# Kernel tuning notes

Measured on AMD Instinct MI355X. Metric: run time of the kernel, lower is better.

Reference implementation:

```python
import jax, jax.numpy as jnp
import numpy as np

IN, U = 256, 512
UNFOLDS = 6

def setup_inputs() -> dict:
    key = jax.random.key(0)
    ks = jax.random.split(key, 16)
    B = 512
    inputs = jax.random.normal(ks[0], (B, IN), dtype=jnp.float32)
    state = jax.random.normal(ks[1], (B, U), dtype=jnp.float32)
    # parameters, initialized like the torch module
    sensory_mu = jax.random.uniform(ks[2], (IN, U), minval=0.3, maxval=0.8)
    sensory_sigma = jax.random.uniform(ks[3], (IN, U), minval=3.0, maxval=8.0)
    sensory_W = jax.random.uniform(ks[4], (IN, U), minval=0.01, maxval=1.0)
    sensory_erev = (2.0 * jax.random.randint(ks[5], (IN, U), 0, 2).astype(jnp.float32) - 1.0)
    mu = jax.random.uniform(ks[6], (U, U), minval=0.3, maxval=0.8)
    sigma = jax.random.uniform(ks[7], (U, U), minval=3.0, maxval=8.0)
    W = jax.random.uniform(ks[8], (U, U), minval=0.01, maxval=1.0)
    erev = (2.0 * jax.random.randint(ks[9], (U, U), 0, 2).astype(jnp.float32) - 1.0)
    vleak = jax.random.uniform(ks[10], (U,), minval=-0.2, maxval=0.2)
    gleak = jnp.ones((U,), dtype=jnp.float32)   # gleak_init_min == max == 1.0
    cm_t = jnp.full((U,), 0.5, dtype=jnp.float32)  # cm_init_min == max == 0.5
    input_w = jnp.ones((IN,), dtype=jnp.float32)
    input_b = jnp.zeros((IN,), dtype=jnp.float32)
    return dict(inputs=inputs, state=state, input_w=input_w, input_b=input_b,
                sensory_mu=sensory_mu, sensory_sigma=sensory_sigma,
                sensory_W=sensory_W, sensory_erev=sensory_erev,
                mu=mu, sigma=sigma, W=W, erev=erev,
                vleak=vleak, gleak=gleak, cm_t=cm_t)

def _syn_sigmoid(v, mu, sigma):
    # v: [B, N] -> [B, N, 1]; mu, sigma: [N, M]; result [B, N, M]
    return jax.nn.sigmoid(sigma * (v[..., None] - mu))

def reference(inputs, state, input_w, input_b, sensory_mu, sensory_sigma,
              sensory_W, sensory_erev, mu, sigma, W, erev, vleak, gleak, cm_t):
    # Affine input mapping
    x = inputs * input_w + input_b                       # [B, IN]
    # sensory synapses (computed once)
    sens_act = sensory_W * _syn_sigmoid(x, sensory_mu, sensory_sigma)  # [B, IN, U]
    w_num_s = jnp.sum(sens_act * sensory_erev, axis=1)   # [B, U]
    w_den_s = jnp.sum(sens_act, axis=1)                  # [B, U]
    # semi-implicit ODE unfold (6 fixed steps)
    v_pre = state
    for _ in range(UNFOLDS):
        w_act = W * _syn_sigmoid(v_pre, mu, sigma)       # [B, U, U]
        w_num = jnp.sum(w_act * erev, axis=1) + w_num_s  # [B, U]
        w_den = jnp.sum(w_act, axis=1) + w_den_s         # [B, U]
        numerator = cm_t * v_pre + gleak * vleak + w_num
        denominator = cm_t + gleak + w_den
        v_pre = numerator / denominator
    return v_pre  # module returns (next_state, next_state); both identical
```

## Files before the change

kernel.cpp:

```cpp
#include <hip/hip_runtime.h>

#define IN_DIM 256
#define U_DIM  512
#define L2E    1.44269504088896340736f

__global__ void k_fuse(const float* __restrict__ mu, const float* __restrict__ sigma,
                       const float* __restrict__ W, const float* __restrict__ erev,
                       float2* __restrict__ sm2, float* __restrict__ wep, int n) {
    int i = blockIdx.x * blockDim.x + threadIdx.x;
    if (i < n) {
        float s = sigma[i] * L2E;
        sm2[i] = make_float2(s, mu[i] * s);
        wep[i] = W[i] * erev[i];
    }
}

__global__ __launch_bounds__(512, 4) void k_sensory(
    const float* __restrict__ inputs, const float* __restrict__ input_w,
    const float* __restrict__ input_b,
    const float* __restrict__ smu, const float* __restrict__ ssig,
    const float* __restrict__ sW, const float* __restrict__ serev,
    float* __restrict__ wnum_s, float* __restrict__ wden_s) {
    __shared__ __align__(16) float xs[8 * IN_DIM];
    __shared__ float red[8 * 8 * 64 * 2];
    const int tid = threadIdx.x;
    const int b0 = blockIdx.x * 8;
    const int u0 = blockIdx.y * 64;

    #pragma unroll
    for (int k = 0; k < 4; ++k) {
        int idx = tid + k * 512;
        int r = idx >> 8, i = idx & 255;
        xs[idx] = fmaf(inputs[(b0 + r) * IN_DIM + i], input_w[i], input_b[i]);
    }
    __syncthreads();

    const int ul = tid & 63;
    const int strip = tid >> 6;
    const int u = u0 + ul;
    float nacc[8], dacc[8];
    #pragma unroll
    for (int r = 0; r < 8; ++r) { nacc[r] = 0.f; dacc[r] = 0.f; }

    const int i0 = strip * 32;
    for (int ic = 0; ic < 32; ic += 4) {
        const int i = i0 + ic;
        float sgl[4], msl[4], w_[4], wer[4];
        #pragma unroll
        for (int j = 0; j < 4; ++j) {
            const int pi = (i + j) * U_DIM + u;
            float m = smu[pi];
            float sg = ssig[pi] * L2E;
            float w = sW[pi];
            sgl[j] = sg; msl[j] = m * sg; w_[j] = w; wer[j] = w * serev[pi];
        }
        #pragma unroll
        for (int r = 0; r < 8; ++r) {
            const float4 x4 = *reinterpret_cast<const float4*>(&xs[r * IN_DIM + i]);
            const float xv[4] = { x4.x, x4.y, x4.z, x4.w };
            #pragma unroll
            for (int j = 0; j < 4; ++j) {
                float e = __builtin_amdgcn_exp2f(fmaf(-sgl[j], xv[j], msl[j]));
                float p = __builtin_amdgcn_rcpf(1.f + e);
                nacc[r] = fmaf(wer[j], p, nacc[r]);
                dacc[r] = fmaf(w_[j], p, dacc[r]);
            }
        }
    }
    #pragma unroll
    for (int r = 0; r < 8; ++r) {
        red[(((strip * 8 + r) * 64) + ul) * 2 + 0] = nacc[r];
        red[(((strip * 8 + r) * 64) + ul) * 2 + 1] = dacc[r];
    }
    __syncthreads();
    {
        const int r = tid >> 6, uu = tid & 63;
        float n = 0.f, d = 0.f;
        #pragma unroll
        for (int s = 0; s < 8; ++s) {
            n += red[(((s * 8 + r) * 64) + uu) * 2 + 0];
            d += red[(((s * 8 + r) * 64) + uu) * 2 + 1];
        }
        wnum_s[(b0 + r) * U_DIM + (u0 + uu)] = n;
        wden_s[(b0 + r) * U_DIM + (u0 + uu)] = d;
    }
}

__global__ __launch_bounds__(512, 4) void k_unfold(
    const float* __restrict__ vin,
    const float2* __restrict__ sm2, const float* __restrict__ wep,
    const float* __restrict__ wnum_s, const float* __restrict__ wden_s,
    const float* __restrict__ vleak, const float* __restrict__ gleak,
    const float* __restrict__ cm,
    float* __restrict__ vout) {
    __shared__ __align__(16) float vs[8 * U_DIM];
    __shared__ float red[8 * 8 * 64 * 2];
    const int tid = threadIdx.x;
    const int b0 = blockIdx.x * 8;
    const int u0 = blockIdx.y * 64;

    #pragma unroll
    for (int k = 0; k < 8; ++k) {
        int idx = tid + k * 512;
        vs[idx] = vin[b0 * U_DIM + idx];
    }
    __syncthreads();

    const int ul = tid & 63;
    const int strip = tid >> 6;
    const int u = u0 + ul;
    float nacc[8], dacc[8];
    #pragma unroll
    for (int r = 0; r < 8; ++r) { nacc[r] = 0.f; dacc[r] = 0.f; }

    const int i0 = strip * 64;
    for (int ic = 0; ic < 64; ic += 4) {
        const int i = i0 + ic;
        float2 p0 = sm2[(i + 0) * U_DIM + u];
        float2 p1 = sm2[(i + 1) * U_DIM + u];
        float2 p2 = sm2[(i + 2) * U_DIM + u];
        float2 p3 = sm2[(i + 3) * U_DIM + u];
        float we0 = wep[(i + 0) * U_DIM + u];
        float we1 = wep[(i + 1) * U_DIM + u];
        float we2 = wep[(i + 2) * U_DIM + u];
        float we3 = wep[(i + 3) * U_DIM + u];
        float w0 = fabsf(we0), w1 = fabsf(we1), w2 = fabsf(we2), w3 = fabsf(we3);
        #pragma unroll
        for (int r = 0; r < 8; ++r) {
            const float4 v4 = *reinterpret_cast<const float4*>(&vs[r * U_DIM + i]);
            {
                float e = __builtin_amdgcn_exp2f(fmaf(-p0.x, v4.x, p0.y));
                float p = __builtin_amdgcn_rcpf(1.f + e);
                nacc[r] = fmaf(we0, p, nacc[r]); dacc[r] = fmaf(w0, p, dacc[r]);
            }
            {
                float e = __builtin_amdgcn_exp2f(fmaf(-p1.x, v4.y, p1.y));
                float p = __builtin_amdgcn_rcpf(1.f + e);
                nacc[r] = fmaf(we1, p, nacc[r]); dacc[r] = fmaf(w1, p, dacc[r]);
            }
            {
                float e = __builtin_amdgcn_exp2f(fmaf(-p2.x, v4.z, p2.y));
                float p = __builtin_amdgcn_rcpf(1.f + e);
                nacc[r] = fmaf(we2, p, nacc[r]); dacc[r] = fmaf(w2, p, dacc[r]);
            }
            {
                float e = __builtin_amdgcn_exp2f(fmaf(-p3.x, v4.w, p3.y));
                float p = __builtin_amdgcn_rcpf(1.f + e);
                nacc[r] = fmaf(we3, p, nacc[r]); dacc[r] = fmaf(w3, p, dacc[r]);
            }
        }
    }
    #pragma unroll
    for (int r = 0; r < 8; ++r) {
        red[(((strip * 8 + r) * 64) + ul) * 2 + 0] = nacc[r];
        red[(((strip * 8 + r) * 64) + ul) * 2 + 1] = dacc[r];
    }
    __syncthreads();
    {
        const int r = tid >> 6, uu = tid & 63;
        float n = 0.f, d = 0.f;
        #pragma unroll
        for (int s = 0; s < 8; ++s) {
            n += red[(((s * 8 + r) * 64) + uu) * 2 + 0];
            d += red[(((s * 8 + r) * 64) + uu) * 2 + 1];
        }
        const int gu = u0 + uu, gb = b0 + r;
        float vold = vs[r * U_DIM + gu];
        float gl = gleak[gu], c = cm[gu];
        float num = fmaf(c, vold, fmaf(gl, vleak[gu], n + wnum_s[gb * U_DIM + gu]));
        float den = c + gl + d + wden_s[gb * U_DIM + gu];
        vout[gb * U_DIM + gu] = num / den;
    }
}

__global__ __launch_bounds__(512) void k_mono(
    const float* __restrict__ inputs, const float* __restrict__ state,
    const float* __restrict__ input_w, const float* __restrict__ input_b,
    const float* __restrict__ smu, const float* __restrict__ ssig,
    const float* __restrict__ sW, const float* __restrict__ serev,
    const float* __restrict__ mu, const float* __restrict__ sigma,
    const float* __restrict__ W, const float* __restrict__ erev,
    const float* __restrict__ vleak, const float* __restrict__ gleak,
    const float* __restrict__ cm, float* __restrict__ out) {
    __shared__ float xs[IN_DIM];
    __shared__ float vsh[U_DIM];
    const int b = blockIdx.x, u = threadIdx.x;
    if (u < IN_DIM) xs[u] = fmaf(inputs[b * IN_DIM + u], input_w[u], input_b[u]);
    vsh[u] = state[b * U_DIM + u];
    __syncthreads();
    float ns = 0.f, ds = 0.f;
    for (int i = 0; i < IN_DIM; ++i) {
        int pi = i * U_DIM + u;
        float e = __builtin_amdgcn_exp2f((smu[pi] - xs[i]) * (ssig[pi] * L2E));
        float p = __builtin_amdgcn_rcpf(1.f + e);
        float a = sW[pi] * p;
        ns = fmaf(a, serev[pi], ns);
        ds += a;
    }
    const float c = cm[u], gl = gleak[u], glvl = gl * vleak[u];
    for (int t = 0; t < 6; ++t) {
        float n = ns, d = ds;
        for (int i = 0; i < U_DIM; ++i) {
            int pi = i * U_DIM + u;
            float e = __builtin_amdgcn_exp2f((mu[pi] - vsh[i]) * (sigma[pi] * L2E));
            float p = __builtin_amdgcn_rcpf(1.f + e);
            float a = W[pi] * p;
            n = fmaf(a, erev[pi], n);
            d += a;
        }
        float vn = (fmaf(c, vsh[u], glvl) + n) / (c + gl + d);
        __syncthreads();
        vsh[u] = vn;
        __syncthreads();
    }
    out[b * U_DIM + u] = vsh[u];
}

extern "C" void kernel_launch(void* const* d_in, const int* in_sizes, int n_in,
                              void* d_out, int out_size, void* d_ws, size_t ws_size,
                              hipStream_t stream) {
    const float* inputs  = (const float*)d_in[0];
    const float* state   = (const float*)d_in[1];
    const float* input_w = (const float*)d_in[2];
    const float* input_b = (const float*)d_in[3];
    const float* smu     = (const float*)d_in[4];
    const float* ssig    = (const float*)d_in[5];
    const float* sW      = (const float*)d_in[6];
    const float* serev   = (const float*)d_in[7];
    const float* mu      = (const float*)d_in[8];
    const float* sigma   = (const float*)d_in[9];
    const float* W       = (const float*)d_in[10];
    const float* erev    = (const float*)d_in[11];
    const float* vleak   = (const float*)d_in[12];
    const float* gleak   = (const float*)d_in[13];
    const float* cm      = (const float*)d_in[14];
    float* out = (float*)d_out;

    const int B = in_sizes[1] / U_DIM;
    const size_t BU = (size_t)B * U_DIM;
    const size_t UU = (size_t)U_DIM * U_DIM;
    const size_t need = (3 * BU + 3 * UU) * sizeof(float);

    if (ws_size >= need) {
        float* f      = (float*)d_ws;
        float* wnum_s = f;
        float* wden_s = f + BU;
        float* vbuf   = f + 2 * BU;
        float2* sm2   = (float2*)(f + 3 * BU);
        float* wep    = f + 3 * BU + 2 * UU;

        k_fuse<<<(int)((UU + 255) / 256), 256, 0, stream>>>(mu, sigma, W, erev, sm2, wep, (int)UU);
        dim3 grid(B / 8, U_DIM / 64);
        k_sensory<<<grid, 512, 0, stream>>>(inputs, input_w, input_b,
                                            smu, ssig, sW, serev, wnum_s, wden_s);
        const float* vin = state;
        float* pong[2] = { vbuf, out };
        for (int t = 0; t < 6; ++t) {
            float* vo = pong[t & 1];
            k_unfold<<<grid, 512, 0, stream>>>(vin, sm2, wep,
                                               wnum_s, wden_s, vleak, gleak, cm, vo);
            vin = vo;
        }
    } else {
        k_mono<<<B, U_DIM, 0, stream>>>(inputs, state, input_w, input_b,
                                        smu, ssig, sW, serev, mu, sigma, W, erev,
                                        vleak, gleak, cm, out);
    }
}
```

Before: 220.2 us.

## Pack synapse params into float4, shrink batch tile to 4, raise occupancy

Precomputes both the recurrent and the sensory synapse parameters into interleaved float4 records (scaled sigma, mu*sigma, W*erev, W), so each inner step issues one 16-byte load. The sensory kernel now reads these records instead of recomputing them from four arrays. Both compute kernels drop their batch tile from 8 to 4 rows and raise the launch bounds to 8 blocks per SM, for more blocks and occupancy. The cost is parameter reuse across rows halving, so twice as many parameter loads per unit of work, plus a larger workspace and a bigger preprocessing kernel.

```diff
diff --git a/kernel.cpp b/kernel.cpp
--- a/kernel.cpp
+++ b/kernel.cpp
@@ -6,29 +6,36 @@
 
 __global__ void k_fuse(const float* __restrict__ mu, const float* __restrict__ sigma,
                        const float* __restrict__ W, const float* __restrict__ erev,
-                       float2* __restrict__ sm2, float* __restrict__ wep, int n) {
+                       const float* __restrict__ smu, const float* __restrict__ ssig,
+                       const float* __restrict__ sW, const float* __restrict__ serev,
+                       float4* __restrict__ pf4, float4* __restrict__ sf4) {
     int i = blockIdx.x * blockDim.x + threadIdx.x;
-    if (i < n) {
+    const int UU = U_DIM * U_DIM;
+    const int SU = IN_DIM * U_DIM;
+    if (i < UU) {
         float s = sigma[i] * L2E;
-        sm2[i] = make_float2(s, mu[i] * s);
-        wep[i] = W[i] * erev[i];
-    }
-}
-
-__global__ __launch_bounds__(512, 4) void k_sensory(
+        float w = W[i];
+        pf4[i] = make_float4(s, mu[i] * s, w * erev[i], w);
+    } else if (i < UU + SU) {
+        int j = i - UU;
+        float s = ssig[j] * L2E;
+        float w = sW[j];
+        sf4[j] = make_float4(s, smu[j] * s, w * serev[j], w);
+    }
+}
+
+__global__ __launch_bounds__(512, 8) void k_sensory(
     const float* __restrict__ inputs, const float* __restrict__ input_w,
-    const float* __restrict__ input_b,
-    const float* __restrict__ smu, const float* __restrict__ ssig,
-    const float* __restrict__ sW, const float* __restrict__ serev,
+    const float* __restrict__ input_b, const float4* __restrict__ sf4,
     float* __restrict__ wnum_s, float* __restrict__ wden_s) {
-    __shared__ __align__(16) float xs[8 * IN_DIM];
-    __shared__ float red[8 * 8 * 64 * 2];
+    __shared__ __align__(16) float xs[4 * IN_DIM];
+    __shared__ float red[8 * 4 * 64 * 2];
     const int tid = threadIdx.x;
-    const int b0 = blockIdx.x * 8;
+    const int b0 = blockIdx.x * 4;
     const int u0 = blockIdx.y * 64;
 
     #pragma unroll
-    for (int k = 0; k < 4; ++k) {
+    for (int k = 0; k < 2; ++k) {
         int idx = tid + k * 512;
         int r = idx >> 8, i = idx & 255;
         xs[idx] = fmaf(inputs[(b0 + r) * IN_DIM + i], input_w[i], input_b[i]);
@@ -38,131 +45,128 @@
     const int ul = tid & 63;
     const int strip = tid >> 6;
     const int u = u0 + ul;
-    float nacc[8], dacc[8];
-    #pragma unroll
-    for (int r = 0; r < 8; ++r) { nacc[r] = 0.f; dacc[r] = 0.f; }
+    float nacc[4], dacc[4];
+    #pragma unroll
+    for (int r = 0; r < 4; ++r) { nacc[r] = 0.f; dacc[r] = 0.f; }
 
     const int i0 = strip * 32;
     for (int ic = 0; ic < 32; ic += 4) {
         const int i = i0 + ic;
-        float sgl[4], msl[4], w_[4], wer[4];
-        #pragma unroll
-        for (int j = 0; j < 4; ++j) {
-            const int pi = (i + j) * U_DIM + u;
-            float m = smu[pi];
-            float sg = ssig[pi] * L2E;
-            float w = sW[pi];
-            sgl[j] = sg; msl[j] = m * sg; w_[j] = w; wer[j] = w * serev[pi];
-        }
-        #pragma unroll
-        for (int r = 0; r < 8; ++r) {
+        float4 q0 = sf4[(i + 0) * U_DIM + u];
+        float4 q1 = sf4[(i + 1) * U_DIM + u];
+        float4 q2 = sf4[(i + 2) * U_DIM + u];
+        float4 q3 = sf4[(i + 3) * U_DIM + u];
+        #pragma unroll
+        for (int r = 0; r < 4; ++r) {
             const float4 x4 = *reinterpret_cast<const float4*>(&xs[r * IN_DIM + i]);
-            const float xv[4] = { x4.x, x4.y, x4.z, x4.w };
-            #pragma unroll
-            for (int j = 0; j < 4; ++j) {
-                float e = __builtin_amdgcn_exp2f(fmaf(-sgl[j], xv[j], msl[j]));
-                float p = __builtin_amdgcn_rcpf(1.f + e);
-                nacc[r] = fmaf(wer[j], p, nacc[r]);
-                dacc[r] = fmaf(w_[j], p, dacc[r]);
-            }
-        }
-    }
-    #pragma unroll
-    for (int r = 0; r < 8; ++r) {
-        red[(((strip * 8 + r) * 64) + ul) * 2 + 0] = nacc[r];
-        red[(((strip * 8 + r) * 64) + ul) * 2 + 1] = dacc[r];
-    }
-    __syncthreads();
-    {
+            {
+                float e = __builtin_amdgcn_exp2f(fmaf(-q0.x, x4.x, q0.y));
+                float p = __builtin_amdgcn_rcpf(1.f + e);
+                nacc[r] = fmaf(q0.z, p, nacc[r]); dacc[r] = fmaf(q0.w, p, dacc[r]);
+            }
+            {
+                float e = __builtin_amdgcn_exp2f(fmaf(-q1.x, x4.y, q1.y));
+                float p = __builtin_amdgcn_rcpf(1.f + e);
+                nacc[r] = fmaf(q1.z, p, nacc[r]); dacc[r] = fmaf(q1.w, p, dacc[r]);
+            }
+            {
+                float e = __builtin_amdgcn_exp2f(fmaf(-q2.x, x4.z, q2.y));
+                float p = __builtin_amdgcn_rcpf(1.f + e);
+                nacc[r] = fmaf(q2.z, p, nacc[r]); dacc[r] = fmaf(q2.w, p, dacc[r]);
+            }
+            {
+                float e = __builtin_amdgcn_exp2f(fmaf(-q3.x, x4.w, q3.y));
+                float p = __builtin_amdgcn_rcpf(1.f + e);
+                nacc[r] = fmaf(q3.z, p, nacc[r]); dacc[r] = fmaf(q3.w, p, dacc[r]);
+            }
+        }
+    }
+    #pragma unroll
+    for (int r = 0; r < 4; ++r) {
+        red[(((strip * 4 + r) * 64) + ul) * 2 + 0] = nacc[r];
+        red[(((strip * 4 + r) * 64) + ul) * 2 + 1] = dacc[r];
+    }
+    __syncthreads();
+    if (tid < 4 * 64) {
         const int r = tid >> 6, uu = tid & 63;
         float n = 0.f, d = 0.f;
         #pragma unroll
         for (int s = 0; s < 8; ++s) {
-            n += red[(((s * 8 + r) * 64) + uu) * 2 + 0];
-            d += red[(((s * 8 + r) * 64) + uu) * 2 + 1];
+            n += red[(((s * 4 + r) * 64) + uu) * 2 + 0];
+            d += red[(((s * 4 + r) * 64) + uu) * 2 + 1];
         }
         wnum_s[(b0 + r) * U_DIM + (u0 + uu)] = n;
         wden_s[(b0 + r) * U_DIM + (u0 + uu)] = d;
     }
 }
 
-__global__ __launch_bounds__(512, 4) void k_unfold(
-    const float* __restrict__ vin,
-    const float2* __restrict__ sm2, const float* __restrict__ wep,
+__global__ __launch_bounds__(512, 8) void k_unfold(
+    const float* __restrict__ vin, const float4* __restrict__ pf4,
     const float* __restrict__ wnum_s, const float* __restrict__ wden_s,
     const float* __restrict__ vleak, const float* __restrict__ gleak,
-    const float* __restrict__ cm,
-    float* __restrict__ vout) {
-    __shared__ __align__(16) float vs[8 * U_DIM];
-    __shared__ float red[8 * 8 * 64 * 2];
+    const float* __restrict__ cm, float* __restrict__ vout) {
+    __shared__ __align__(16) float vs[4 * U_DIM];
+    __shared__ float red[8 * 4 * 64 * 2];
     const int tid = threadIdx.x;
-    const int b0 = blockIdx.x * 8;
+    const int b0 = blockIdx.x * 4;
     const int u0 = blockIdx.y * 64;
 
-    #pragma unroll
-    for (int k = 0; k < 8; ++k) {
-        int idx = tid + k * 512;
-        vs[idx] = vin[b0 * U_DIM + idx];
-    }
+    reinterpret_cast<float4*>(vs)[tid] =
+        reinterpret_cast<const float4*>(vin + (size_t)b0 * U_DIM)[tid];
     __syncthreads();
 
     const int ul = tid & 63;
     const int strip = tid >> 6;
     const int u = u0 + ul;
-    float nacc[8], dacc[8];
-    #pragma unroll
-    for (int r = 0; r < 8; ++r) { nacc[r] = 0.f; dacc[r] = 0.f; }
+    float nacc[4], dacc[4];
+    #pragma unroll
+    for (int r = 0; r < 4; ++r) { nacc[r] = 0.f; dacc[r] = 0.f; }
 
     const int i0 = strip * 64;
     for (int ic = 0; ic < 64; ic += 4) {
         const int i = i0 + ic;
-        float2 p0 = sm2[(i + 0) * U_DIM + u];
-        float2 p1 = sm2[(i + 1) * U_DIM + u];
-        float2 p2 = sm2[(i + 2) * U_DIM + u];
-        float2 p3 = sm2[(i + 3) * U_DIM + u];
-        float we0 = wep[(i + 0) * U_DIM + u];
-        float we1 = wep[(i + 1) * U_DIM + u];
-        float we2 = wep[(i + 2) * U_DIM + u];
-        float we3 = wep[(i + 3) * U_DIM + u];
-        float w0 = fabsf(we0), w1 = fabsf(we1), w2 = fabsf(we2), w3 = fabsf(we3);
-        #pragma unroll
-        for (int r = 0; r < 8; ++r) {
+        float4 q0 = pf4[(i + 0) * U_DIM + u];
+        float4 q1 = pf4[(i + 1) * U_DIM + u];
+        float4 q2 = pf4[(i + 2) * U_DIM + u];
+        float4 q3 = pf4[(i + 3) * U_DIM + u];
+        #pragma unroll
+        for (int r = 0; r < 4; ++r) {
             const float4 v4 = *reinterpret_cast<const float4*>(&vs[r * U_DIM + i]);
             {
-                float e = __builtin_amdgcn_exp2f(fmaf(-p0.x, v4.x, p0.y));
-                float p = __builtin_amdgcn_rcpf(1.f + e);
-                nacc[r] = fmaf(we0, p, nacc[r]); dacc[r] = fmaf(w0, p, dacc[r]);
-            }
-            {
-                float e = __builtin_amdgcn_exp2f(fmaf(-p1.x, v4.y, p1.y));
-                float p = __builtin_amdgcn_rcpf(1.f + e);
-                nacc[r] = fmaf(we1, p, nacc[r]); dacc[r] = fmaf(w1, p, dacc[r]);
-            }
-            {
-                float e = __builtin_amdgcn_exp2f(fmaf(-p2.x, v4.z, p2.y));
-                float p = __builtin_amdgcn_rcpf(1.f + e);
-                nacc[r] = fmaf(we2, p, nacc[r]); dacc[r] = fmaf(w2, p, dacc[r]);
-            }
-            {
-                float e = __builtin_amdgcn_exp2f(fmaf(-p3.x, v4.w, p3.y));
-                float p = __builtin_amdgcn_rcpf(1.f + e);
-                nacc[r] = fmaf(we3, p, nacc[r]); dacc[r] = fmaf(w3, p, dacc[r]);
-            }
-        }
-    }
-    #pragma unroll
-    for (int r = 0; r < 8; ++r) {
-        red[(((strip * 8 + r) * 64) + ul) * 2 + 0] = nacc[r];
-        red[(((strip * 8 + r) * 64) + ul) * 2 + 1] = dacc[r];
-    }
-    __syncthreads();
-    {
+                float e = __builtin_amdgcn_exp2f(fmaf(-q0.x, v4.x, q0.y));
+                float p = __builtin_amdgcn_rcpf(1.f + e);
+                nacc[r] = fmaf(q0.z, p, nacc[r]); dacc[r] = fmaf(q0.w, p, dacc[r]);
+            }
+            {
+                float e = __builtin_amdgcn_exp2f(fmaf(-q1.x, v4.y, q1.y));
+                float p = __builtin_amdgcn_rcpf(1.f + e);
+                nacc[r] = fmaf(q1.z, p, nacc[r]); dacc[r] = fmaf(q1.w, p, dacc[r]);
+            }
+            {
+                float e = __builtin_amdgcn_exp2f(fmaf(-q2.x, v4.z, q2.y));
+                float p = __builtin_amdgcn_rcpf(1.f + e);
+                nacc[r] = fmaf(q2.z, p, nacc[r]); dacc[r] = fmaf(q2.w, p, dacc[r]);
+            }
+            {
+                float e = __builtin_amdgcn_exp2f(fmaf(-q3.x, v4.w, q3.y));
+                float p = __builtin_amdgcn_rcpf(1.f + e);
+                nacc[r] = fmaf(q3.z, p, nacc[r]); dacc[r] = fmaf(q3.w, p, dacc[r]);
+            }
+        }
+    }
+    #pragma unroll
+    for (int r = 0; r < 4; ++r) {
+        red[(((strip * 4 + r) * 64) + ul) * 2 + 0] = nacc[r];
+        red[(((strip * 4 + r) * 64) + ul) * 2 + 1] = dacc[r];
+    }
+    __syncthreads();
+    if (tid < 4 * 64) {
         const int r = tid >> 6, uu = tid & 63;
         float n = 0.f, d = 0.f;
         #pragma unroll
         for (int s = 0; s < 8; ++s) {
-            n += red[(((s * 8 + r) * 64) + uu) * 2 + 0];
-            d += red[(((s * 8 + r) * 64) + uu) * 2 + 1];
+            n += red[(((s * 4 + r) * 64) + uu) * 2 + 0];
+            d += red[(((s * 4 + r) * 64) + uu) * 2 + 1];
         }
         const int gu = u0 + uu, gb = b0 + r;
         float vold = vs[r * U_DIM + gu];
@@ -239,26 +243,28 @@
     const int B = in_sizes[1] / U_DIM;
     const size_t BU = (size_t)B * U_DIM;
     const size_t UU = (size_t)U_DIM * U_DIM;
-    const size_t need = (3 * BU + 3 * UU) * sizeof(float);
+    const size_t SU = (size_t)IN_DIM * U_DIM;
+    const size_t need = (3 * BU + 4 * UU + 4 * SU) * sizeof(float);
 
     if (ws_size >= need) {
         float* f      = (float*)d_ws;
         float* wnum_s = f;
         float* wden_s = f + BU;
         float* vbuf   = f + 2 * BU;
-        float2* sm2   = (float2*)(f + 3 * BU);
-        float* wep    = f + 3 * BU + 2 * UU;
-
-        k_fuse<<<(int)((UU + 255) / 256), 256, 0, stream>>>(mu, sigma, W, erev, sm2, wep, (int)UU);
-        dim3 grid(B / 8, U_DIM / 64);
-        k_sensory<<<grid, 512, 0, stream>>>(inputs, input_w, input_b,
-                                            smu, ssig, sW, serev, wnum_s, wden_s);
+        float4* pf4   = (float4*)(f + 3 * BU);
+        float4* sf4   = (float4*)(f + 3 * BU + 4 * UU);
+
+        const int nfuse = (int)(UU + SU);
+        k_fuse<<<(nfuse + 255) / 256, 256, 0, stream>>>(mu, sigma, W, erev,
+                                                        smu, ssig, sW, serev, pf4, sf4);
+        dim3 grid(B / 4, U_DIM / 64);
+        k_sensory<<<grid, 512, 0, stream>>>(inputs, input_w, input_b, sf4, wnum_s, wden_s);
         const float* vin = state;
         float* pong[2] = { vbuf, out };
         for (int t = 0; t < 6; ++t) {
             float* vo = pong[t & 1];
-            k_unfold<<<grid, 512, 0, stream>>>(vin, sm2, wep,
-                                               wnum_s, wden_s, vleak, gleak, cm, vo);
+            k_unfold<<<grid, 512, 0, stream>>>(vin, pf4, wnum_s, wden_s,
+                                               vleak, gleak, cm, vo);
             vin = vo;
         }
     } else {
```

After: 223.1 us. About the same (+1.3%).

## Pack synapse parameters in pairs for packed-FP32 math and halve unit tile

Applied to the files above, without the earlier changes.

Preprocessing now interleaves parameters for two adjacent presynaptic rows into float4 records (negated scaled sigma, scaled mu, W*erev, W). This lets the inner loops issue one 16-byte load and use two-wide FMAs that can map to packed FP32 instructions. The sensory stage gets the same preprocessing, replacing its per-element parameter loads. Each block now covers 32 units with two strips per wave, combined by a cross-half shuffle before the shared reduction, which doubles the grid. The final division becomes an approximate reciprocal multiply, and the preprocessing pass writes more workspace.

```diff
diff --git a/kernel.cpp b/kernel.cpp
--- a/kernel.cpp
+++ b/kernel.cpp
@@ -4,28 +4,67 @@
 #define U_DIM  512
 #define L2E    1.44269504088896340736f
 
+typedef float f32x2 __attribute__((ext_vector_type(2)));
+typedef float f32x4 __attribute__((ext_vector_type(4)));
+
+__device__ __forceinline__ f32x2 vfma2(f32x2 a, f32x2 b, f32x2 c) {
+    return __builtin_elementwise_fma(a, b, c);
+}
+
 __global__ void k_fuse(const float* __restrict__ mu, const float* __restrict__ sigma,
                        const float* __restrict__ W, const float* __restrict__ erev,
-                       float2* __restrict__ sm2, float* __restrict__ wep, int n) {
-    int i = blockIdx.x * blockDim.x + threadIdx.x;
-    if (i < n) {
-        float s = sigma[i] * L2E;
-        sm2[i] = make_float2(s, mu[i] * s);
-        wep[i] = W[i] * erev[i];
-    }
-}
+                       const float* __restrict__ smu, const float* __restrict__ ssig,
+                       const float* __restrict__ sW, const float* __restrict__ serev,
+                       f32x4* __restrict__ rp4, f32x4* __restrict__ wp4,
+                       f32x4* __restrict__ sp4, f32x4* __restrict__ swp4) {
+    const int NR = (U_DIM / 2) * U_DIM;
+    const int NS = (IN_DIM / 2) * U_DIM;
+    int t = blockIdx.x * blockDim.x + threadIdx.x;
+    if (t < NR) {
+        const int u = t & (U_DIM - 1);
+        const int pr = t >> 9;
+        const int a = (2 * pr) * U_DIM + u, b = (2 * pr + 1) * U_DIM + u;
+        float s0 = sigma[a] * L2E, s1 = sigma[b] * L2E;
+        float w0 = W[a], w1 = W[b];
+        rp4[t] = (f32x4){ -s0, -s1, mu[a] * s0, mu[b] * s1 };
+        wp4[t] = (f32x4){ w0 * erev[a], w1 * erev[b], w0, w1 };
+    } else if (t < NR + NS) {
+        const int j = t - NR;
+        const int u = j & (U_DIM - 1);
+        const int pr = j >> 9;
+        const int a = (2 * pr) * U_DIM + u, b = (2 * pr + 1) * U_DIM + u;
+        float s0 = ssig[a] * L2E, s1 = ssig[b] * L2E;
+        float w0 = sW[a], w1 = sW[b];
+        sp4[j] = (f32x4){ -s0, -s1, smu[a] * s0, smu[b] * s1 };
+        swp4[j] = (f32x4){ w0 * serev[a], w1 * serev[b], w0, w1 };
+    }
+}
+
+#define PAIR_STEP(Q, WD, VP, NA, DA)                                               \
+    {                                                                              \
+        f32x2 t_ = vfma2((Q).xy, (VP), (Q).zw);                                    \
+        f32x2 e_;                                                                  \
+        e_.x = __builtin_amdgcn_exp2f(t_.x);                                       \
+        e_.y = __builtin_amdgcn_exp2f(t_.y);                                       \
+        f32x2 d_ = e_ + (f32x2)(1.f);                                              \
+        f32x2 p_;                                                                  \
+        p_.x = __builtin_amdgcn_rcpf(d_.x);                                        \
+        p_.y = __builtin_amdgcn_rcpf(d_.y);                                        \
+        (NA) = vfma2((WD).xy, p_, (NA));                                           \
+        (DA) = vfma2((WD).zw, p_, (DA));                                           \
+    }
 
 __global__ __launch_bounds__(512, 4) void k_sensory(
     const float* __restrict__ inputs, const float* __restrict__ input_w,
     const float* __restrict__ input_b,
-    const float* __restrict__ smu, const float* __restrict__ ssig,
-    const float* __restrict__ sW, const float* __restrict__ serev,
+    const f32x4* __restrict__ sp4, const f32x4* __restrict__ swp4,
     float* __restrict__ wnum_s, float* __restrict__ wden_s) {
     __shared__ __align__(16) float xs[8 * IN_DIM];
-    __shared__ float red[8 * 8 * 64 * 2];
+    __shared__ float red_n[8 * 8 * 32];
+    __shared__ float red_d[8 * 8 * 32];
     const int tid = threadIdx.x;
     const int b0 = blockIdx.x * 8;
-    const int u0 = blockIdx.y * 64;
+    const int u0 = blockIdx.y * 32;
 
     #pragma unroll
     for (int k = 0; k < 4; ++k) {
@@ -35,141 +74,140 @@
     }
     __syncthreads();
 
-    const int ul = tid & 63;
-    const int strip = tid >> 6;
-    const int u = u0 + ul;
-    float nacc[8], dacc[8];
-    #pragma unroll
-    for (int r = 0; r < 8; ++r) { nacc[r] = 0.f; dacc[r] = 0.f; }
-
+    const int lane = tid & 63;
+    const int w = tid >> 6;
+    const int ulh = lane & 31;
+    const int ih = lane >> 5;
+    const int strip = w * 2 + ih;
+    const int u = u0 + ulh;
+    const int i0 = strip * 16;
+
+    f32x2 nacc[8], dacc[8];
+    #pragma unroll
+    for (int r = 0; r < 8; ++r) { nacc[r] = (f32x2)(0.f); dacc[r] = (f32x2)(0.f); }
+
+    for (int ic = 0; ic < 16; ic += 4) {
+        const int i = i0 + ic;
+        const int pr = i >> 1;
+        f32x4 q0 = sp4[(pr + 0) * U_DIM + u];
+        f32x4 q1 = sp4[(pr + 1) * U_DIM + u];
+        f32x4 w0 = swp4[(pr + 0) * U_DIM + u];
+        f32x4 w1 = swp4[(pr + 1) * U_DIM + u];
+        #pragma unroll
+        for (int r = 0; r < 8; ++r) {
+            const f32x4 v4 = *reinterpret_cast<const f32x4*>(&xs[r * IN_DIM + i]);
+            PAIR_STEP(q0, w0, v4.xy, nacc[r], dacc[r])
+            PAIR_STEP(q1, w1, v4.zw, nacc[r], dacc[r])
+        }
+    }
+
+    float nf[8], df[8];
+    #pragma unroll
+    for (int r = 0; r < 8; ++r) {
+        nf[r] = nacc[r].x + nacc[r].y;
+        df[r] = dacc[r].x + dacc[r].y;
+        nf[r] += __shfl_xor(nf[r], 32);
+        df[r] += __shfl_xor(df[r], 32);
+    }
+    if (lane < 32) {
+        #pragma unroll
+        for (int r = 0; r < 8; ++r) {
+            red_n[(w * 8 + r) * 32 + ulh] = nf[r];
+            red_d[(w * 8 + r) * 32 + ulh] = df[r];
+        }
+    }
+    __syncthreads();
+    if (tid < 8 * 32) {
+        const int r = tid >> 5, uu = tid & 31;
+        float n = 0.f, d = 0.f;
+        #pragma unroll
+        for (int s = 0; s < 8; ++s) {
+            n += red_n[(s * 8 + r) * 32 + uu];
+            d += red_d[(s * 8 + r) * 32 + uu];
+        }
+        wnum_s[(b0 + r) * U_DIM + (u0 + uu)] = n;
+        wden_s[(b0 + r) * U_DIM + (u0 + uu)] = d;
+    }
+}
+
+__global__ __launch_bounds__(512, 4) void k_unfold(
+    const float* __restrict__ vin,
+    const f32x4* __restrict__ rp4, const f32x4* __restrict__ wp4,
+    const float* __restrict__ wnum_s, const float* __restrict__ wden_s,
+    const float* __restrict__ vleak, const float* __restrict__ gleak,
+    const float* __restrict__ cm, float* __restrict__ vout) {
+    __shared__ __align__(16) float vs[8 * U_DIM];
+    __shared__ float red_n[8 * 8 * 32];
+    __shared__ float red_d[8 * 8 * 32];
+    const int tid = threadIdx.x;
+    const int b0 = blockIdx.x * 8;
+    const int u0 = blockIdx.y * 32;
+
+    #pragma unroll
+    for (int k = 0; k < 2; ++k) {
+        int idx = tid + k * 512;
+        reinterpret_cast<float4*>(vs)[idx] =
+            reinterpret_cast<const float4*>(vin + (size_t)b0 * U_DIM)[idx];
+    }
+    __syncthreads();
+
+    const int lane = tid & 63;
+    const int w = tid >> 6;
+    const int ulh = lane & 31;
+    const int ih = lane >> 5;
+    const int strip = w * 2 + ih;
+    const int u = u0 + ulh;
     const int i0 = strip * 32;
+
+    f32x2 nacc[8], dacc[8];
+    #pragma unroll
+    for (int r = 0; r < 8; ++r) { nacc[r] = (f32x2)(0.f); dacc[r] = (f32x2)(0.f); }
+
     for (int ic = 0; ic < 32; ic += 4) {
         const int i = i0 + ic;
-        float sgl[4], msl[4], w_[4], wer[4];
-        #pragma unroll
-        for (int j = 0; j < 4; ++j) {
-            const int pi = (i + j) * U_DIM + u;
-            float m = smu[pi];
-            float sg = ssig[pi] * L2E;
-            float w = sW[pi];
-            sgl[j] = sg; msl[j] = m * sg; w_[j] = w; wer[j] = w * serev[pi];
-        }
+        const int pr = i >> 1;
+        f32x4 q0 = rp4[(pr + 0) * U_DIM + u];
+        f32x4 q1 = rp4[(pr + 1) * U_DIM + u];
+        f32x4 w0 = wp4[(pr + 0) * U_DIM + u];
+        f32x4 w1 = wp4[(pr + 1) * U_DIM + u];
         #pragma unroll
         for (int r = 0; r < 8; ++r) {
-            const float4 x4 = *reinterpret_cast<const float4*>(&xs[r * IN_DIM + i]);
-            const float xv[4] = { x4.x, x4.y, x4.z, x4.w };
-            #pragma unroll
-            for (int j = 0; j < 4; ++j) {
-                float e = __builtin_amdgcn_exp2f(fmaf(-sgl[j], xv[j], msl[j]));
-                float p = __builtin_amdgcn_rcpf(1.f + e);
-                nacc[r] = fmaf(wer[j], p, nacc[r]);
-                dacc[r] = fmaf(w_[j], p, dacc[r]);
-            }
-        }
-    }
+            const f32x4 v4 = *reinterpret_cast<const f32x4*>(&vs[r * U_DIM + i]);
+            PAIR_STEP(q0, w0, v4.xy, nacc[r], dacc[r])
+            PAIR_STEP(q1, w1, v4.zw, nacc[r], dacc[r])
+        }
+    }
+
+    float nf[8], df[8];
     #pragma unroll
     for (int r = 0; r < 8; ++r) {
-        red[(((strip * 8 + r) * 64) + ul) * 2 + 0] = nacc[r];
-        red[(((strip * 8 + r) * 64) + ul) * 2 + 1] = dacc[r];
-    }
-    __syncthreads();
-    {
-        const int r = tid >> 6, uu = tid & 63;
+        nf[r] = nacc[r].x + nacc[r].y;
+        df[r] = dacc[r].x + dacc[r].y;
+        nf[r] += __shfl_xor(nf[r], 32);
+        df[r] += __shfl_xor(df[r], 32);
+    }
+    if (lane < 32) {
+        #pragma unroll
+        for (int r = 0; r < 8; ++r) {
+            red_n[(w * 8 + r) * 32 + ulh] = nf[r];
+            red_d[(w * 8 + r) * 32 + ulh] = df[r];
+        }
+    }
+    __syncthreads();
+    if (tid < 8 * 32) {
+        const int r = tid >> 5, uu = tid & 31;
         float n = 0.f, d = 0.f;
         #pragma unroll
         for (int s = 0; s < 8; ++s) {
-            n += red[(((s * 8 + r) * 64) + uu) * 2 + 0];
-            d += red[(((s * 8 + r) * 64) + uu) * 2 + 1];
-        }
-        wnum_s[(b0 + r) * U_DIM + (u0 + uu)] = n;
-        wden_s[(b0 + r) * U_DIM + (u0 + uu)] = d;
-    }
-}
-
-__global__ __launch_bounds__(512, 4) void k_unfold(
-    const float* __restrict__ vin,
-    const float2* __restrict__ sm2, const float* __restrict__ wep,
-    const float* __restrict__ wnum_s, const float* __restrict__ wden_s,
-    const float* __restrict__ vleak, const float* __restrict__ gleak,
-    const float* __restrict__ cm,
-    float* __restrict__ vout) {
-    __shared__ __align__(16) float vs[8 * U_DIM];
-    __shared__ float red[8 * 8 * 64 * 2];
-    const int tid = threadIdx.x;
-    const int b0 = blockIdx.x * 8;
-    const int u0 = blockIdx.y * 64;
-
-    #pragma unroll
-    for (int k = 0; k < 8; ++k) {
-        int idx = tid + k * 512;
-        vs[idx] = vin[b0 * U_DIM + idx];
-    }
-    __syncthreads();
-
-    const int ul = tid & 63;
-    const int strip = tid >> 6;
-    const int u = u0 + ul;
-    float nacc[8], dacc[8];
-    #pragma unroll
-    for (int r = 0; r < 8; ++r) { nacc[r] = 0.f; dacc[r] = 0.f; }
-
-    const int i0 = strip * 64;
-    for (int ic = 0; ic < 64; ic += 4) {
-        const int i = i0 + ic;
-        float2 p0 = sm2[(i + 0) * U_DIM + u];
-        float2 p1 = sm2[(i + 1) * U_DIM + u];
-        float2 p2 = sm2[(i + 2) * U_DIM + u];
-        float2 p3 = sm2[(i + 3) * U_DIM + u];
-        float we0 = wep[(i + 0) * U_DIM + u];
-        float we1 = wep[(i + 1) * U_DIM + u];
-        float we2 = wep[(i + 2) * U_DIM + u];
-        float we3 = wep[(i + 3) * U_DIM + u];
-        float w0 = fabsf(we0), w1 = fabsf(we1), w2 = fabsf(we2), w3 = fabsf(we3);
-        #pragma unroll
-        for (int r = 0; r < 8; ++r) {
-            const float4 v4 = *reinterpret_cast<const float4*>(&vs[r * U_DIM + i]);
-            {
-                float e = __builtin_amdgcn_exp2f(fmaf(-p0.x, v4.x, p0.y));
-                float p = __builtin_amdgcn_rcpf(1.f + e);
-                nacc[r] = fmaf(we0, p, nacc[r]); dacc[r] = fmaf(w0, p, dacc[r]);
-            }
-            {
-                float e = __builtin_amdgcn_exp2f(fmaf(-p1.x, v4.y, p1.y));
-                float p = __builtin_amdgcn_rcpf(1.f + e);
-                nacc[r] = fmaf(we1, p, nacc[r]); dacc[r] = fmaf(w1, p, dacc[r]);
-            }
-            {
-                float e = __builtin_amdgcn_exp2f(fmaf(-p2.x, v4.z, p2.y));
-                float p = __builtin_amdgcn_rcpf(1.f + e);
-                nacc[r] = fmaf(we2, p, nacc[r]); dacc[r] = fmaf(w2, p, dacc[r]);
-            }
-            {
-                float e = __builtin_amdgcn_exp2f(fmaf(-p3.x, v4.w, p3.y));
-                float p = __builtin_amdgcn_rcpf(1.f + e);
-                nacc[r] = fmaf(we3, p, nacc[r]); dacc[r] = fmaf(w3, p, dacc[r]);
-            }
-        }
-    }
-    #pragma unroll
-    for (int r = 0; r < 8; ++r) {
-        red[(((strip * 8 + r) * 64) + ul) * 2 + 0] = nacc[r];
-        red[(((strip * 8 + r) * 64) + ul) * 2 + 1] = dacc[r];
-    }
-    __syncthreads();
-    {
-        const int r = tid >> 6, uu = tid & 63;
-        float n = 0.f, d = 0.f;
-        #pragma unroll
-        for (int s = 0; s < 8; ++s) {
-            n += red[(((s * 8 + r) * 64) + uu) * 2 + 0];
-            d += red[(((s * 8 + r) * 64) + uu) * 2 + 1];
+            n += red_n[(s * 8 + r) * 32 + uu];
+            d += red_d[(s * 8 + r) * 32 + uu];
         }
         const int gu = u0 + uu, gb = b0 + r;
         float vold = vs[r * U_DIM + gu];
         float gl = gleak[gu], c = cm[gu];
         float num = fmaf(c, vold, fmaf(gl, vleak[gu], n + wnum_s[gb * U_DIM + gu]));
         float den = c + gl + d + wden_s[gb * U_DIM + gu];
-        vout[gb * U_DIM + gu] = num / den;
+        vout[gb * U_DIM + gu] = num * __builtin_amdgcn_rcpf(den);
     }
 }
 
@@ -239,26 +277,32 @@
     const int B = in_sizes[1] / U_DIM;
     const size_t BU = (size_t)B * U_DIM;
     const size_t UU = (size_t)U_DIM * U_DIM;
-    const size_t need = (3 * BU + 3 * UU) * sizeof(float);
+    const size_t SU = (size_t)IN_DIM * U_DIM;
+    const size_t need = (3 * BU + 4 * UU + 4 * SU) * sizeof(float);
 
     if (ws_size >= need) {
         float* f      = (float*)d_ws;
         float* wnum_s = f;
         float* wden_s = f + BU;
         float* vbuf   = f + 2 * BU;
-        float2* sm2   = (float2*)(f + 3 * BU);
-        float* wep    = f + 3 * BU + 2 * UU;
-
-        k_fuse<<<(int)((UU + 255) / 256), 256, 0, stream>>>(mu, sigma, W, erev, sm2, wep, (int)UU);
-        dim3 grid(B / 8, U_DIM / 64);
-        k_sensory<<<grid, 512, 0, stream>>>(inputs, input_w, input_b,
-                                            smu, ssig, sW, serev, wnum_s, wden_s);
+        f32x4* rp4    = (f32x4*)(f + 3 * BU);
+        f32x4* wp4    = (f32x4*)(f + 3 * BU + 2 * UU);
+        f32x4* sp4    = (f32x4*)(f + 3 * BU + 4 * UU);
+        f32x4* swp4   = (f32x4*)(f + 3 * BU + 4 * UU + 2 * SU);
+
+        const int nfuse = (int)(UU / 2 + SU / 2);
+        k_fuse<<<(nfuse + 255) / 256, 256, 0, stream>>>(mu, sigma, W, erev,
+                                                        smu, ssig, sW, serev,
+                                                        rp4, wp4, sp4, swp4);
+        dim3 grid(B / 8, U_DIM / 32);
+        k_sensory<<<grid, 512, 0, stream>>>(inputs, input_w, input_b, sp4, swp4,
+                                            wnum_s, wden_s);
         const float* vin = state;
         float* pong[2] = { vbuf, out };
         for (int t = 0; t < 6; ++t) {
             float* vo = pong[t & 1];
-            k_unfold<<<grid, 512, 0, stream>>>(vin, sm2, wep,
-                                               wnum_s, wden_s, vleak, gleak, cm, vo);
+            k_unfold<<<grid, 512, 0, stream>>>(vin, rp4, wp4, wnum_s, wden_s,
+                                               vleak, gleak, cm, vo);
             vin = vo;
         }
     } else {
```

Result: faster. 206.9 us (-6.0%).
